# Kernel tuning notes

Measured on AMD Instinct MI355X. Metric: run time of the kernel, lower is better.

Reference implementation:

```python
import jax, jax.numpy as jnp
import numpy as np
import math

B, S, D, H = 32, 512, 1024, 1024


def setup_inputs() -> dict:
    key = jax.random.key(0)
    k_feats, k_wih, k_whh, k_bih, k_bhh = jax.random.split(key, 5)
    stdv = 1.0 / math.sqrt(H)
    u = lambda k, shape: jax.random.uniform(k, shape, jnp.float32, -stdv, stdv)
    return {
        "feats": jax.random.normal(k_feats, (B, S, D), jnp.float32),
        "weight_ih": u(k_wih, (3 * H, D)),
        "weight_hh": u(k_whh, (3 * H, H)),
        "bias_ih": u(k_bih, (3 * H,)),
        "bias_hh": u(k_bhh, (3 * H,)),
    }


def reference(feats, weight_ih, weight_hh, bias_ih, bias_hh):
    b, s, d = feats.shape
    h_dim = weight_hh.shape[1]
    # Precompute input projections for all timesteps in one GEMM: [B,S,3H]
    gi_all = jnp.einsum('bsd,gd->bsg', feats, weight_ih) + bias_ih

    def step(h, gi_t):
        gh = h @ weight_hh.T + bias_hh  # [B,3H]
        i_r, i_i, i_n = jnp.split(gi_t, 3, axis=-1)
        h_r, h_i, h_n = jnp.split(gh, 3, axis=-1)
        resetgate = jax.nn.sigmoid(i_r + h_r)
        inputgate = jax.nn.sigmoid(i_i + h_i)
        newgate = jnp.tanh(i_n + resetgate * h_n)
        hy = newgate + inputgate * (h - newgate)
        return hy, hy

    h0 = jnp.zeros((b, h_dim), feats.dtype)
    h_last, outs = jax.lax.scan(step, h0, jnp.swapaxes(gi_all, 0, 1))  # outs: [S,B,H]
    output = jnp.swapaxes(outs, 0, 1)  # [B,S,H]
    return output, h_last
```

## Files before the change

kernel.cpp:

```cpp
#include <hip/hip_runtime.h>

#define B_  32
#define S_  512
#define D_  1024
#define H_  1024
#define G3  3072

typedef __attribute__((ext_vector_type(8))) short  short8;
typedef __attribute__((ext_vector_type(4))) float  floatx4;

__device__ __forceinline__ unsigned short f2bf(float f) {
    unsigned int u = __builtin_bit_cast(unsigned int, f);
    u = (u + 0x7FFFu + ((u >> 16) & 1u)) >> 16;
    return (unsigned short)u;
}
__device__ __forceinline__ float bf2f(unsigned short h) {
    unsigned int u = ((unsigned int)h) << 16;
    return __builtin_bit_cast(float, u);
}
__device__ __forceinline__ float fsigmoid(float x) {
    float e = __builtin_amdgcn_exp2f(-1.4426950408889634f * x);
    return __builtin_amdgcn_rcpf(1.f + e);
}
__device__ __forceinline__ float ftanh(float x) {
    float e = __builtin_amdgcn_exp2f(2.8853900817779268f * x);
    return 1.f - 2.f * __builtin_amdgcn_rcpf(e + 1.f);
}

__global__ __launch_bounds__(256) void convert_kernel(
    const float* __restrict__ wih, const float* __restrict__ whh,
    unsigned short* __restrict__ wih_h,
    unsigned short* __restrict__ whh_h, unsigned short* __restrict__ whh_l,
    unsigned int* __restrict__ hbuf ,
    int* __restrict__ cnt ) {
    int tid = blockIdx.x * 256 + threadIdx.x;
    int i4 = tid * 4;
    if (i4 < 3145728) {
        float4 w = *(const float4*)(wih + i4);
        ushort4 o;
        o.x = f2bf(w.x); o.y = f2bf(w.y); o.z = f2bf(w.z); o.w = f2bf(w.w);
        *(ushort4*)(wih_h + i4) = o;

        float4 v = *(const float4*)(whh + i4);
        ushort4 h;
        h.x = f2bf(v.x); h.y = f2bf(v.y); h.z = f2bf(v.z); h.w = f2bf(v.w);
        ushort4 l;
        l.x = f2bf(v.x - bf2f(h.x)); l.y = f2bf(v.y - bf2f(h.y));
        l.z = f2bf(v.z - bf2f(h.z)); l.w = f2bf(v.w - bf2f(h.w));
        *(ushort4*)(whh_h + i4) = h;
        *(ushort4*)(whh_l + i4) = l;
    }
    if (tid < 16384) {
        uint4 z; z.x = z.y = z.z = z.w = 0;
        *(uint4*)(hbuf + tid * 4) = z;
    }
    if (tid < 32) {
        int4 z4; z4.x = z4.y = z4.z = z4.w = 0;
        *(int4*)(cnt + tid * 4) = z4;
    }
}

#define BM 128
#define BN 128
#define BK 32
#define LDA 40

__global__ __launch_bounds__(256, 2) void gi_gemm(
    const float* __restrict__ feats,
    const unsigned short* __restrict__ wih_h,
    const float* __restrict__ bias_ih,
    unsigned short* __restrict__ gi) {
    __shared__ unsigned short As[BM * LDA];
    __shared__ unsigned short Bs[BN * LDA];

    int bx = blockIdx.x;
    int nb = bx % (G3 / BN);
    int mb = bx / (G3 / BN);
    int m0 = mb * BM, n0 = nb * BN;
    int tid = threadIdx.x;
    int lane = tid & 63, wave = tid >> 6;
    int quad = lane >> 4, l15 = lane & 15;
    int wm = (wave >> 1) * 64, wn = (wave & 1) * 64;

    floatx4 acc[4][4];
#pragma unroll
    for (int i = 0; i < 4; ++i)
#pragma unroll
        for (int j = 0; j < 4; ++j) acc[i][j] = (floatx4){0.f, 0.f, 0.f, 0.f};

    float bias[4];
#pragma unroll
    for (int j = 0; j < 4; ++j) bias[j] = bias_ih[n0 + wn + j * 16 + l15];

    int srow = tid >> 1, shalf = tid & 1;
    const float* aptr = feats + (size_t)(m0 + srow) * D_ + shalf * 16;
    const unsigned short* bptr = wih_h + (size_t)(n0 + srow) * D_ + shalf * 16;
    unsigned short* as = As + srow * LDA + shalf * 16;
    unsigned short* bs = Bs + srow * LDA + shalf * 16;

    for (int kt = 0; kt < D_ / BK; ++kt) {
        int k0 = kt * BK;
        float4 a0 = *(const float4*)(aptr + k0);
        float4 a1 = *(const float4*)(aptr + k0 + 4);
        float4 a2 = *(const float4*)(aptr + k0 + 8);
        float4 a3 = *(const float4*)(aptr + k0 + 12);
        uint4 bA = *(const uint4*)(bptr + k0);
        uint4 bB = *(const uint4*)(bptr + k0 + 8);

        union { unsigned short u16[16]; uint4 v[2]; } pk;
        pk.u16[0] = f2bf(a0.x);  pk.u16[1] = f2bf(a0.y);
        pk.u16[2] = f2bf(a0.z);  pk.u16[3] = f2bf(a0.w);
        pk.u16[4] = f2bf(a1.x);  pk.u16[5] = f2bf(a1.y);
        pk.u16[6] = f2bf(a1.z);  pk.u16[7] = f2bf(a1.w);
        pk.u16[8] = f2bf(a2.x);  pk.u16[9] = f2bf(a2.y);
        pk.u16[10] = f2bf(a2.z); pk.u16[11] = f2bf(a2.w);
        pk.u16[12] = f2bf(a3.x); pk.u16[13] = f2bf(a3.y);
        pk.u16[14] = f2bf(a3.z); pk.u16[15] = f2bf(a3.w);

        *(uint4*)as = pk.v[0];
        *(uint4*)(as + 8) = pk.v[1];
        *(uint4*)bs = bA;
        *(uint4*)(bs + 8) = bB;
        __syncthreads();

        short8 af[4], bf[4];
#pragma unroll
        for (int i = 0; i < 4; ++i)
            af[i] = *(const short8*)(As + (wm + i * 16 + l15) * LDA + quad * 8);
#pragma unroll
        for (int j = 0; j < 4; ++j)
            bf[j] = *(const short8*)(Bs + (wn + j * 16 + l15) * LDA + quad * 8);
#pragma unroll
        for (int i = 0; i < 4; ++i)
#pragma unroll
            for (int j = 0; j < 4; ++j)
                acc[i][j] = __builtin_amdgcn_mfma_f32_16x16x32_bf16(
                    af[i], bf[j], acc[i][j], 0, 0, 0);
        __syncthreads();
    }

#pragma unroll
    for (int i = 0; i < 4; ++i)
#pragma unroll
        for (int j = 0; j < 4; ++j)
#pragma unroll
            for (int r = 0; r < 4; ++r) {
                int m = m0 + wm + i * 16 + quad * 4 + r;
                int n = n0 + wn + j * 16 + l15;
                gi[(size_t)m * G3 + n] = f2bf(acc[i][j][r] + bias[j]);
            }
}

__global__ __launch_bounds__(512, 2) void gru_rec(
    const unsigned short* __restrict__ gi,
    const unsigned short* __restrict__ whh_h,
    const unsigned short* __restrict__ whh_l,
    const float* __restrict__ bias_hh,
    unsigned int* __restrict__ hbuf,
    int* __restrict__ cnt,
    float* __restrict__ out) {
    __shared__ floatx4 parts[8][3][64];

    int jg = blockIdx.x >> 1, mt = blockIdx.x & 1;
    int tid = threadIdx.x;
    int ks = tid >> 6, lane = tid & 63;
    int quad = lane >> 4, l15 = lane & 15;
    int j = jg * 16 + l15;

    short8 wfh[3][4], wfl[3][4];
#pragma unroll
    for (int g = 0; g < 3; ++g)
#pragma unroll
        for (int ki = 0; ki < 4; ++ki) {
            size_t off = (size_t)(g * H_ + j) * H_ + ks * 128 + ki * 32 + quad * 8;
            wfh[g][ki] = *(const short8*)(whh_h + off);
            wfl[g][ki] = *(const short8*)(whh_l + off);
        }

    float bhh[3] = {0.f, 0.f, 0.f};
    float hreg[4] = {0.f, 0.f, 0.f, 0.f};
    if (ks == 0) {
#pragma unroll
        for (int g = 0; g < 3; ++g) bhh[g] = bias_hh[g * H_ + j];
    }

    const int arow = mt * 16 + l15;
    const int kbase = ks * 128 + quad * 8;
    int* const cbase = cnt + mt * 64;

    for (int t = 0; t < S_; ++t) {
        unsigned short giu[3][4];
        if (ks == 0) {
#pragma unroll
            for (int g = 0; g < 3; ++g)
#pragma unroll
                for (int r = 0; r < 4; ++r) {
                    int b = mt * 16 + quad * 4 + r;
                    giu[g][r] = gi[((size_t)b * S_ + t) * G3 + g * H_ + j];
                }
        }

        if (t > 0) {
            if (ks == 0) {
                int v = __hip_atomic_load(cbase + lane, __ATOMIC_RELAXED,
                                          __HIP_MEMORY_SCOPE_AGENT);
                while (!__all(v >= t)) {
                    __builtin_amdgcn_s_sleep(1);
                    v = __hip_atomic_load(cbase + lane, __ATOMIC_RELAXED,
                                          __HIP_MEMORY_SCOPE_AGENT);
                }
            }
            __syncthreads();
        }

        const unsigned int* hc = hbuf + ((t & 1) << 15);
        unsigned int* hn = hbuf + (((t & 1) ^ 1) << 15);

        unsigned long long q[16];
        {
            const unsigned long long* p =
                (const unsigned long long*)(hc + arow * H_ + kbase);
#pragma unroll
            for (int ki = 0; ki < 4; ++ki)
#pragma unroll
                for (int c = 0; c < 4; ++c)
                    q[ki * 4 + c] = __hip_atomic_load(p + ki * 16 + c,
                                                      __ATOMIC_RELAXED,
                                                      __HIP_MEMORY_SCOPE_AGENT);
        }
        short8 ah[4], al[4];
#pragma unroll
        for (int ki = 0; ki < 4; ++ki) {
            short8 av, lv;
#pragma unroll
            for (int c = 0; c < 4; ++c) {
                unsigned long long qq = q[ki * 4 + c];
                unsigned int u0 = (unsigned int)qq;
                unsigned int u1 = (unsigned int)(qq >> 32);
                av[2 * c]     = (short)(u0 & 0xffffu);
                av[2 * c + 1] = (short)(u1 & 0xffffu);
                lv[2 * c]     = (short)(u0 >> 16);
                lv[2 * c + 1] = (short)(u1 >> 16);
            }
            ah[ki] = av;
            al[ki] = lv;
        }

        floatx4 acc[3];
#pragma unroll
        for (int g = 0; g < 3; ++g) acc[g] = (floatx4){0.f, 0.f, 0.f, 0.f};
#pragma unroll
        for (int ki = 0; ki < 4; ++ki)
#pragma unroll
            for (int g = 0; g < 3; ++g) {
                acc[g] = __builtin_amdgcn_mfma_f32_16x16x32_bf16(ah[ki], wfh[g][ki], acc[g], 0, 0, 0);
                acc[g] = __builtin_amdgcn_mfma_f32_16x16x32_bf16(ah[ki], wfl[g][ki], acc[g], 0, 0, 0);
                acc[g] = __builtin_amdgcn_mfma_f32_16x16x32_bf16(al[ki], wfh[g][ki], acc[g], 0, 0, 0);
            }
#pragma unroll
        for (int g = 0; g < 3; ++g) parts[ks][g][lane] = acc[g];
        __syncthreads();

        float hy[4];
        if (ks == 0) {
            floatx4 gh[3];
#pragma unroll
            for (int g = 0; g < 3; ++g) {
                floatx4 s = parts[0][g][lane];
#pragma unroll
                for (int w = 1; w < 8; ++w) s += parts[w][g][lane];
                gh[g] = s;
            }
#pragma unroll
            for (int r = 0; r < 4; ++r) {
                int b = mt * 16 + quad * 4 + r;
                float rg = fsigmoid(bf2f(giu[0][r]) + gh[0][r] + bhh[0]);
                float zg = fsigmoid(bf2f(giu[1][r]) + gh[1][r] + bhh[1]);
                float ng = ftanh(bf2f(giu[2][r]) + rg * (gh[2][r] + bhh[2]));
                float h = ng + zg * (hreg[r] - ng);
                hreg[r] = h;
                hy[r] = h;
                unsigned short hh = f2bf(h);
                unsigned int pk = (unsigned int)hh |
                                  ((unsigned int)f2bf(h - bf2f(hh)) << 16);
                __hip_atomic_store(hn + b * H_ + j, pk, __ATOMIC_RELAXED,
                                   __HIP_MEMORY_SCOPE_AGENT);
            }
            asm volatile("s_waitcnt vmcnt(0)" ::: "memory");
            if (tid == 0)
                __hip_atomic_store(cbase + jg, t + 1, __ATOMIC_RELAXED,
                                   __HIP_MEMORY_SCOPE_AGENT);
#pragma unroll
            for (int r = 0; r < 4; ++r) {
                int b = mt * 16 + quad * 4 + r;
                __builtin_nontemporal_store(hy[r], out + ((size_t)b * S_ + t) * H_ + j);
                if (t == S_ - 1)
                    __builtin_nontemporal_store(hy[r], out + (size_t)B_ * S_ * H_ + (size_t)b * H_ + j);
            }
        }
    }
}

extern "C" void kernel_launch(void* const* d_in, const int* in_sizes, int n_in,
                              void* d_out, int out_size, void* d_ws, size_t ws_size,
                              hipStream_t stream) {
    const float* feats = (const float*)d_in[0];
    const float* wih   = (const float*)d_in[1];
    const float* whh   = (const float*)d_in[2];
    const float* bih   = (const float*)d_in[3];
    const float* bhh   = (const float*)d_in[4];
    float* out = (float*)d_out;

    unsigned short* wih_h = (unsigned short*)d_ws;
    unsigned short* whh_h = wih_h + (size_t)3145728;
    unsigned short* whh_l = whh_h + (size_t)3145728;
    unsigned short* gi    = whh_l + (size_t)3145728;
    unsigned int*   hbuf  = (unsigned int*)(gi + (size_t)16384 * G3);
    int*            cnt   = (int*)(hbuf + 65536);

    hipLaunchKernelGGL(convert_kernel, dim3(3072), dim3(256), 0, stream,
                       wih, whh, wih_h, whh_h, whh_l, hbuf, cnt);
    hipLaunchKernelGGL(gi_gemm, dim3(3072), dim3(256), 0, stream,
                       feats, wih_h, bih, gi);

    void* args[] = {(void*)&gi, (void*)&whh_h, (void*)&whh_l,
                    (void*)&bhh, (void*)&hbuf, (void*)&cnt, (void*)&out};
    hipLaunchCooperativeKernel((const void*)gru_rec, dim3(128), dim3(512),
                               args, 0, stream);
}
```

Before: 3.435 ms.

## Replace counter barrier with step-tagged hidden-state words and spread gate epilogue

Drops the per-block progress counters and the spin-wait-then-syncthreads handshake. Each hidden-state entry is now stored as a 64-bit word carrying the timestep tag beside the packed bf16 hi/lo value. Consumers poll their own slice until every tag matches, and they do it in two halves so the MFMA inputs for the first half can be ready sooner. The gate epilogue now runs on 256 threads with one element each instead of one wave handling four, and the next step's gi values are prefetched during the current step. The cost is twice the hidden-state traffic per step and an extra __syncthreads.

```diff
diff --git a/kernel.cpp b/kernel.cpp
--- a/kernel.cpp
+++ b/kernel.cpp
@@ -31,8 +31,7 @@
     const float* __restrict__ wih, const float* __restrict__ whh,
     unsigned short* __restrict__ wih_h,
     unsigned short* __restrict__ whh_h, unsigned short* __restrict__ whh_l,
-    unsigned int* __restrict__ hbuf ,
-    int* __restrict__ cnt ) {
+    unsigned int* __restrict__ hbuf ) {
     int tid = blockIdx.x * 256 + threadIdx.x;
     int i4 = tid * 4;
     if (i4 < 3145728) {
@@ -50,13 +49,9 @@
         *(ushort4*)(whh_h + i4) = h;
         *(ushort4*)(whh_l + i4) = l;
     }
-    if (tid < 16384) {
+    if (tid < 32768) {
         uint4 z; z.x = z.y = z.z = z.w = 0;
         *(uint4*)(hbuf + tid * 4) = z;
-    }
-    if (tid < 32) {
-        int4 z4; z4.x = z4.y = z4.z = z4.w = 0;
-        *(int4*)(cnt + tid * 4) = z4;
     }
 }
 
@@ -156,16 +151,15 @@
     const unsigned short* __restrict__ whh_h,
     const unsigned short* __restrict__ whh_l,
     const float* __restrict__ bias_hh,
-    unsigned int* __restrict__ hbuf,
-    int* __restrict__ cnt,
+    unsigned long long* __restrict__ hbuf,
     float* __restrict__ out) {
     __shared__ floatx4 parts[8][3][64];
 
-    int jg = blockIdx.x >> 1, mt = blockIdx.x & 1;
-    int tid = threadIdx.x;
-    int ks = tid >> 6, lane = tid & 63;
-    int quad = lane >> 4, l15 = lane & 15;
-    int j = jg * 16 + l15;
+    const int tid = threadIdx.x;
+    const int lane = tid & 63, ks = tid >> 6;
+    const int quad = lane >> 4, l15 = lane & 15;
+    const int jg = blockIdx.x >> 1, mt = blockIdx.x & 1;
+    const int j = jg * 16 + l15;
 
     short8 wfh[3][4], wfl[3][4];
 #pragma unroll
@@ -177,73 +171,87 @@
             wfl[g][ki] = *(const short8*)(whh_l + off);
         }
 
-    float bhh[3] = {0.f, 0.f, 0.f};
-    float hreg[4] = {0.f, 0.f, 0.f, 0.f};
-    if (ks == 0) {
-#pragma unroll
-        for (int g = 0; g < 3; ++g) bhh[g] = bias_hh[g * H_ + j];
+    const int rr = (tid >> 4) & 15, cc = tid & 15;
+    const int brow = mt * 16 + rr;
+    const int jc = jg * 16 + cc;
+    float bR = 0.f, bZ = 0.f, bN = 0.f, hreg = 0.f;
+    unsigned short giR = 0, giZ = 0, giN = 0;
+    if (tid < 256) {
+        bR = bias_hh[jc]; bZ = bias_hh[H_ + jc]; bN = bias_hh[2 * H_ + jc];
+        const size_t gb = (size_t)brow * S_ * G3 + jc;
+        giR = gi[gb]; giZ = gi[gb + H_]; giN = gi[gb + 2 * H_];
     }
 
     const int arow = mt * 16 + l15;
-    const int kbase = ks * 128 + quad * 8;
-    int* const cbase = cnt + mt * 64;
+    const size_t lslice = (size_t)arow * 1024 + ks * 128 + quad * 8;
+    const float* const pf = (const float*)parts;
 
     for (int t = 0; t < S_; ++t) {
-        unsigned short giu[3][4];
-        if (ks == 0) {
-#pragma unroll
-            for (int g = 0; g < 3; ++g)
-#pragma unroll
-                for (int r = 0; r < 4; ++r) {
-                    int b = mt * 16 + quad * 4 + r;
-                    giu[g][r] = gi[((size_t)b * S_ + t) * G3 + g * H_ + j];
+        const unsigned long long* hp = hbuf + ((size_t)(t & 1) << 15) + lslice;
+        const unsigned int want = (unsigned int)t;
+
+        short8 ah[4], al[4];
+        {
+            unsigned long long q[16];
+            int ok;
+            do {
+#pragma unroll
+                for (int ki = 0; ki < 2; ++ki)
+#pragma unroll
+                    for (int c = 0; c < 8; ++c)
+                        q[ki * 8 + c] = __hip_atomic_load(hp + ki * 32 + c,
+                                                          __ATOMIC_RELAXED,
+                                                          __HIP_MEMORY_SCOPE_AGENT);
+                ok = 1;
+#pragma unroll
+                for (int i = 0; i < 16; ++i)
+                    ok &= ((unsigned int)(q[i] >> 32) == want);
+            } while (!__all(ok));
+#pragma unroll
+            for (int ki = 0; ki < 2; ++ki) {
+                short8 av, lv;
+#pragma unroll
+                for (int c = 0; c < 8; ++c) {
+                    unsigned int d = (unsigned int)q[ki * 8 + c];
+                    av[c] = (short)(d & 0xffffu);
+                    lv[c] = (short)(d >> 16);
                 }
-        }
-
-        if (t > 0) {
-            if (ks == 0) {
-                int v = __hip_atomic_load(cbase + lane, __ATOMIC_RELAXED,
-                                          __HIP_MEMORY_SCOPE_AGENT);
-                while (!__all(v >= t)) {
-                    __builtin_amdgcn_s_sleep(1);
-                    v = __hip_atomic_load(cbase + lane, __ATOMIC_RELAXED,
-                                          __HIP_MEMORY_SCOPE_AGENT);
+                ah[ki] = av; al[ki] = lv;
+            }
+        }
+        {
+            unsigned long long q[16];
+            int ok;
+            do {
+#pragma unroll
+                for (int ki = 0; ki < 2; ++ki)
+#pragma unroll
+                    for (int c = 0; c < 8; ++c)
+                        q[ki * 8 + c] = __hip_atomic_load(hp + (ki + 2) * 32 + c,
+                                                          __ATOMIC_RELAXED,
+                                                          __HIP_MEMORY_SCOPE_AGENT);
+                ok = 1;
+#pragma unroll
+                for (int i = 0; i < 16; ++i)
+                    ok &= ((unsigned int)(q[i] >> 32) == want);
+            } while (!__all(ok));
+#pragma unroll
+            for (int ki = 0; ki < 2; ++ki) {
+                short8 av, lv;
+#pragma unroll
+                for (int c = 0; c < 8; ++c) {
+                    unsigned int d = (unsigned int)q[ki * 8 + c];
+                    av[c] = (short)(d & 0xffffu);
+                    lv[c] = (short)(d >> 16);
                 }
-            }
-            __syncthreads();
-        }
-
-        const unsigned int* hc = hbuf + ((t & 1) << 15);
-        unsigned int* hn = hbuf + (((t & 1) ^ 1) << 15);
-
-        unsigned long long q[16];
-        {
-            const unsigned long long* p =
-                (const unsigned long long*)(hc + arow * H_ + kbase);
-#pragma unroll
-            for (int ki = 0; ki < 4; ++ki)
-#pragma unroll
-                for (int c = 0; c < 4; ++c)
-                    q[ki * 4 + c] = __hip_atomic_load(p + ki * 16 + c,
-                                                      __ATOMIC_RELAXED,
-                                                      __HIP_MEMORY_SCOPE_AGENT);
-        }
-        short8 ah[4], al[4];
-#pragma unroll
-        for (int ki = 0; ki < 4; ++ki) {
-            short8 av, lv;
-#pragma unroll
-            for (int c = 0; c < 4; ++c) {
-                unsigned long long qq = q[ki * 4 + c];
-                unsigned int u0 = (unsigned int)qq;
-                unsigned int u1 = (unsigned int)(qq >> 32);
-                av[2 * c]     = (short)(u0 & 0xffffu);
-                av[2 * c + 1] = (short)(u1 & 0xffffu);
-                lv[2 * c]     = (short)(u0 >> 16);
-                lv[2 * c + 1] = (short)(u1 >> 16);
-            }
-            ah[ki] = av;
-            al[ki] = lv;
+                ah[ki + 2] = av; al[ki + 2] = lv;
+            }
+        }
+
+        unsigned short nR = 0, nZ = 0, nN = 0;
+        if (tid < 256 && t + 1 < S_) {
+            const size_t gb = ((size_t)brow * S_ + (t + 1)) * G3 + jc;
+            nR = gi[gb]; nZ = gi[gb + H_]; nN = gi[gb + 2 * H_];
         }
 
         floatx4 acc[3];
@@ -261,43 +269,39 @@
         for (int g = 0; g < 3; ++g) parts[ks][g][lane] = acc[g];
         __syncthreads();
 
-        float hy[4];
-        if (ks == 0) {
-            floatx4 gh[3];
-#pragma unroll
-            for (int g = 0; g < 3; ++g) {
-                floatx4 s = parts[0][g][lane];
-#pragma unroll
-                for (int w = 1; w < 8; ++w) s += parts[w][g][lane];
-                gh[g] = s;
-            }
-#pragma unroll
-            for (int r = 0; r < 4; ++r) {
-                int b = mt * 16 + quad * 4 + r;
-                float rg = fsigmoid(bf2f(giu[0][r]) + gh[0][r] + bhh[0]);
-                float zg = fsigmoid(bf2f(giu[1][r]) + gh[1][r] + bhh[1]);
-                float ng = ftanh(bf2f(giu[2][r]) + rg * (gh[2][r] + bhh[2]));
-                float h = ng + zg * (hreg[r] - ng);
-                hreg[r] = h;
-                hy[r] = h;
-                unsigned short hh = f2bf(h);
-                unsigned int pk = (unsigned int)hh |
-                                  ((unsigned int)f2bf(h - bf2f(hh)) << 16);
-                __hip_atomic_store(hn + b * H_ + j, pk, __ATOMIC_RELAXED,
-                                   __HIP_MEMORY_SCOPE_AGENT);
-            }
-            asm volatile("s_waitcnt vmcnt(0)" ::: "memory");
-            if (tid == 0)
-                __hip_atomic_store(cbase + jg, t + 1, __ATOMIC_RELAXED,
-                                   __HIP_MEMORY_SCOPE_AGENT);
-#pragma unroll
-            for (int r = 0; r < 4; ++r) {
-                int b = mt * 16 + quad * 4 + r;
-                __builtin_nontemporal_store(hy[r], out + ((size_t)b * S_ + t) * H_ + j);
-                if (t == S_ - 1)
-                    __builtin_nontemporal_store(hy[r], out + (size_t)B_ * S_ * H_ + (size_t)b * H_ + j);
-            }
-        }
+        float gh0 = 0.f, gh1 = 0.f, gh2 = 0.f;
+        if (tid < 256) {
+            const int vidx = ((rr >> 2) * 16 + cc) * 4 + (rr & 3);
+#pragma unroll
+            for (int w = 0; w < 8; ++w) {
+                gh0 += pf[((w * 3 + 0) * 64) * 4 + vidx];
+                gh1 += pf[((w * 3 + 1) * 64) * 4 + vidx];
+                gh2 += pf[((w * 3 + 2) * 64) * 4 + vidx];
+            }
+        }
+        __syncthreads();
+
+        if (tid < 256) {
+            const float rg = fsigmoid(bf2f(giR) + gh0 + bR);
+            const float zg = fsigmoid(bf2f(giZ) + gh1 + bZ);
+            const float ng = ftanh(bf2f(giN) + rg * (gh2 + bN));
+            const float hy = ng + zg * (hreg - ng);
+            hreg = hy;
+            const unsigned short hh = f2bf(hy);
+            const unsigned int pk = (unsigned int)hh |
+                                    ((unsigned int)f2bf(hy - bf2f(hh)) << 16);
+            const unsigned long long hv =
+                ((unsigned long long)(unsigned int)(t + 1) << 32) |
+                (unsigned long long)pk;
+            __hip_atomic_store(hbuf + ((size_t)((t + 1) & 1) << 15) +
+                               (size_t)brow * 1024 + jc,
+                               hv, __ATOMIC_RELAXED, __HIP_MEMORY_SCOPE_AGENT);
+            __builtin_nontemporal_store(hy, out + ((size_t)brow * S_ + t) * H_ + jc);
+            if (t == S_ - 1)
+                __builtin_nontemporal_store(hy,
+                    out + (size_t)B_ * S_ * H_ + (size_t)brow * H_ + jc);
+        }
+        giR = nR; giZ = nZ; giN = nN;
     }
 }
 
@@ -315,16 +319,15 @@
     unsigned short* whh_h = wih_h + (size_t)3145728;
     unsigned short* whh_l = whh_h + (size_t)3145728;
     unsigned short* gi    = whh_l + (size_t)3145728;
-    unsigned int*   hbuf  = (unsigned int*)(gi + (size_t)16384 * G3);
-    int*            cnt   = (int*)(hbuf + 65536);
+    unsigned long long* hbuf = (unsigned long long*)(gi + (size_t)16384 * G3);
 
     hipLaunchKernelGGL(convert_kernel, dim3(3072), dim3(256), 0, stream,
-                       wih, whh, wih_h, whh_h, whh_l, hbuf, cnt);
+                       wih, whh, wih_h, whh_h, whh_l, (unsigned int*)hbuf);
     hipLaunchKernelGGL(gi_gemm, dim3(3072), dim3(256), 0, stream,
                        feats, wih_h, bih, gi);
 
     void* args[] = {(void*)&gi, (void*)&whh_h, (void*)&whh_l,
-                    (void*)&bhh, (void*)&hbuf, (void*)&cnt, (void*)&out};
+                    (void*)&bhh, (void*)&hbuf, (void*)&out};
     hipLaunchCooperativeKernel((const void*)gru_rec, dim3(128), dim3(512),
                                args, 0, stream);
 }
```

New measurement: 5.772 ms. +68.0%, slower.

## Ping-pong two batch halves per block to overlap grid sync with MFMA

Applied to the files above, without the earlier changes.

Each block now owns both 16-row batch halves of its 16 hidden columns, which halves the grid to 64 blocks. It alternates between them: one half's recurrent MFMA runs while the other half's cross-block flag wait is pending, using separate flag arrays and LDS partial buffers. The gate epilogue is spread over 256 threads instead of 64, and output writes are buffered in LDS and flushed every 4 timesteps. Per-block work doubles and is serialized, so the gain depends on hiding spin-wait latency behind the other half's compute.

```diff
diff --git a/kernel.cpp b/kernel.cpp
--- a/kernel.cpp
+++ b/kernel.cpp
@@ -159,13 +159,16 @@
     unsigned int* __restrict__ hbuf,
     int* __restrict__ cnt,
     float* __restrict__ out) {
-    __shared__ floatx4 parts[8][3][64];
-
-    int jg = blockIdx.x >> 1, mt = blockIdx.x & 1;
-    int tid = threadIdx.x;
-    int ks = tid >> 6, lane = tid & 63;
-    int quad = lane >> 4, l15 = lane & 15;
-    int j = jg * 16 + l15;
+    __shared__ floatx4 partsA[8][3][64];
+    __shared__ floatx4 partsB[8][3][64];
+    __shared__ float sbufA[1024];
+    __shared__ float sbufB[1024];
+
+    const int tid = threadIdx.x;
+    const int lane = tid & 63, ks = tid >> 6;
+    const int quad = lane >> 4, l15 = lane & 15;
+    const int jg = blockIdx.x;
+    const int j = jg * 16 + l15;
 
     short8 wfh[3][4], wfl[3][4];
 #pragma unroll
@@ -177,49 +180,36 @@
             wfl[g][ki] = *(const short8*)(whh_l + off);
         }
 
-    float bhh[3] = {0.f, 0.f, 0.f};
-    float hreg[4] = {0.f, 0.f, 0.f, 0.f};
-    if (ks == 0) {
-#pragma unroll
-        for (int g = 0; g < 3; ++g) bhh[g] = bias_hh[g * H_ + j];
-    }
-
-    const int arow = mt * 16 + l15;
+    const int rr = (tid >> 4) & 15, cc = tid & 15;
+    const int browA = rr, browB = 16 + rr;
+    const int jc = jg * 16 + cc;
+    float bR = 0.f, bZ = 0.f, bN = 0.f;
+    float hrA = 0.f, hrB = 0.f;
+    if (tid < 256) {
+        bR = bias_hh[jc]; bZ = bias_hh[H_ + jc]; bN = bias_hh[2 * H_ + jc];
+    }
+
+    int* const fA = cnt;
+    int* const fB = cnt + 64;
     const int kbase = ks * 128 + quad * 8;
-    int* const cbase = cnt + mt * 64;
+    const float* const pfA = (const float*)partsA;
+    const float* const pfB = (const float*)partsB;
 
     for (int t = 0; t < S_; ++t) {
-        unsigned short giu[3][4];
-        if (ks == 0) {
-#pragma unroll
-            for (int g = 0; g < 3; ++g)
-#pragma unroll
-                for (int r = 0; r < 4; ++r) {
-                    int b = mt * 16 + quad * 4 + r;
-                    giu[g][r] = gi[((size_t)b * S_ + t) * G3 + g * H_ + j];
-                }
-        }
-
-        if (t > 0) {
-            if (ks == 0) {
-                int v = __hip_atomic_load(cbase + lane, __ATOMIC_RELAXED,
-                                          __HIP_MEMORY_SCOPE_AGENT);
-                while (!__all(v >= t)) {
-                    __builtin_amdgcn_s_sleep(1);
-                    v = __hip_atomic_load(cbase + lane, __ATOMIC_RELAXED,
-                                          __HIP_MEMORY_SCOPE_AGENT);
-                }
-            }
-            __syncthreads();
-        }
-
         const unsigned int* hc = hbuf + ((t & 1) << 15);
         unsigned int* hn = hbuf + (((t & 1) ^ 1) << 15);
 
-        unsigned long long q[16];
+        unsigned short gAr = 0, gAz = 0, gAn = 0, gBr = 0, gBz = 0, gBn = 0;
+        if (tid < 256) {
+            const size_t gbA = ((size_t)browA * S_ + t) * G3 + jc;
+            const size_t gbB = ((size_t)browB * S_ + t) * G3 + jc;
+            gAr = gi[gbA]; gAz = gi[gbA + H_]; gAn = gi[gbA + 2 * H_];
+            gBr = gi[gbB]; gBz = gi[gbB + H_]; gBn = gi[gbB + 2 * H_];
+        }
         {
+            unsigned long long q[16];
             const unsigned long long* p =
-                (const unsigned long long*)(hc + arow * H_ + kbase);
+                (const unsigned long long*)(hc + (16 + l15) * H_ + kbase);
 #pragma unroll
             for (int ki = 0; ki < 4; ++ki)
 #pragma unroll
@@ -227,77 +217,172 @@
                     q[ki * 4 + c] = __hip_atomic_load(p + ki * 16 + c,
                                                       __ATOMIC_RELAXED,
                                                       __HIP_MEMORY_SCOPE_AGENT);
-        }
-        short8 ah[4], al[4];
-#pragma unroll
-        for (int ki = 0; ki < 4; ++ki) {
-            short8 av, lv;
-#pragma unroll
-            for (int c = 0; c < 4; ++c) {
-                unsigned long long qq = q[ki * 4 + c];
-                unsigned int u0 = (unsigned int)qq;
-                unsigned int u1 = (unsigned int)(qq >> 32);
-                av[2 * c]     = (short)(u0 & 0xffffu);
-                av[2 * c + 1] = (short)(u1 & 0xffffu);
-                lv[2 * c]     = (short)(u0 >> 16);
-                lv[2 * c + 1] = (short)(u1 >> 16);
-            }
-            ah[ki] = av;
-            al[ki] = lv;
-        }
-
-        floatx4 acc[3];
-#pragma unroll
-        for (int g = 0; g < 3; ++g) acc[g] = (floatx4){0.f, 0.f, 0.f, 0.f};
-#pragma unroll
-        for (int ki = 0; ki < 4; ++ki)
-#pragma unroll
-            for (int g = 0; g < 3; ++g) {
-                acc[g] = __builtin_amdgcn_mfma_f32_16x16x32_bf16(ah[ki], wfh[g][ki], acc[g], 0, 0, 0);
-                acc[g] = __builtin_amdgcn_mfma_f32_16x16x32_bf16(ah[ki], wfl[g][ki], acc[g], 0, 0, 0);
-                acc[g] = __builtin_amdgcn_mfma_f32_16x16x32_bf16(al[ki], wfh[g][ki], acc[g], 0, 0, 0);
-            }
-#pragma unroll
-        for (int g = 0; g < 3; ++g) parts[ks][g][lane] = acc[g];
-        __syncthreads();
-
-        float hy[4];
-        if (ks == 0) {
-            floatx4 gh[3];
-#pragma unroll
-            for (int g = 0; g < 3; ++g) {
-                floatx4 s = parts[0][g][lane];
-#pragma unroll
-                for (int w = 1; w < 8; ++w) s += parts[w][g][lane];
-                gh[g] = s;
-            }
-#pragma unroll
-            for (int r = 0; r < 4; ++r) {
-                int b = mt * 16 + quad * 4 + r;
-                float rg = fsigmoid(bf2f(giu[0][r]) + gh[0][r] + bhh[0]);
-                float zg = fsigmoid(bf2f(giu[1][r]) + gh[1][r] + bhh[1]);
-                float ng = ftanh(bf2f(giu[2][r]) + rg * (gh[2][r] + bhh[2]));
-                float h = ng + zg * (hreg[r] - ng);
-                hreg[r] = h;
-                hy[r] = h;
-                unsigned short hh = f2bf(h);
-                unsigned int pk = (unsigned int)hh |
-                                  ((unsigned int)f2bf(h - bf2f(hh)) << 16);
-                __hip_atomic_store(hn + b * H_ + j, pk, __ATOMIC_RELAXED,
-                                   __HIP_MEMORY_SCOPE_AGENT);
-            }
+            short8 ah[4], al[4];
+#pragma unroll
+            for (int ki = 0; ki < 4; ++ki) {
+                short8 av, lv;
+#pragma unroll
+                for (int c = 0; c < 4; ++c) {
+                    unsigned long long qq = q[ki * 4 + c];
+                    unsigned int u0 = (unsigned int)qq;
+                    unsigned int u1 = (unsigned int)(qq >> 32);
+                    av[2 * c]     = (short)(u0 & 0xffffu);
+                    av[2 * c + 1] = (short)(u1 & 0xffffu);
+                    lv[2 * c]     = (short)(u0 >> 16);
+                    lv[2 * c + 1] = (short)(u1 >> 16);
+                }
+                ah[ki] = av; al[ki] = lv;
+            }
+            floatx4 acc[3];
+#pragma unroll
+            for (int g = 0; g < 3; ++g) acc[g] = (floatx4){0.f, 0.f, 0.f, 0.f};
+#pragma unroll
+            for (int ki = 0; ki < 4; ++ki)
+#pragma unroll
+                for (int g = 0; g < 3; ++g) {
+                    acc[g] = __builtin_amdgcn_mfma_f32_16x16x32_bf16(ah[ki], wfh[g][ki], acc[g], 0, 0, 0);
+                    acc[g] = __builtin_amdgcn_mfma_f32_16x16x32_bf16(ah[ki], wfl[g][ki], acc[g], 0, 0, 0);
+                    acc[g] = __builtin_amdgcn_mfma_f32_16x16x32_bf16(al[ki], wfh[g][ki], acc[g], 0, 0, 0);
+                }
+#pragma unroll
+            for (int g = 0; g < 3; ++g) partsB[ks][g][lane] = acc[g];
+        }
+        __syncthreads();
+
+        if (ks == 4) {
+            int v = __hip_atomic_load(fA + lane, __ATOMIC_RELAXED,
+                                      __HIP_MEMORY_SCOPE_AGENT);
+            while (!__all(v >= t)) {
+                __builtin_amdgcn_s_sleep(1);
+                v = __hip_atomic_load(fA + lane, __ATOMIC_RELAXED,
+                                      __HIP_MEMORY_SCOPE_AGENT);
+            }
+        }
+        if (tid < 256) {
+            const int lidx = ((rr >> 2) * 16 + cc);
+            const int r4 = rr & 3;
+            float gh0 = 0.f, gh1 = 0.f, gh2 = 0.f;
+#pragma unroll
+            for (int w = 0; w < 8; ++w) {
+                gh0 += pfB[(((w * 3 + 0) * 64 + lidx) << 2) + r4];
+                gh1 += pfB[(((w * 3 + 1) * 64 + lidx) << 2) + r4];
+                gh2 += pfB[(((w * 3 + 2) * 64 + lidx) << 2) + r4];
+            }
+            const float rg = fsigmoid(bf2f(gBr) + gh0 + bR);
+            const float zg = fsigmoid(bf2f(gBz) + gh1 + bZ);
+            const float ng = ftanh(bf2f(gBn) + rg * (gh2 + bN));
+            const float hy = ng + zg * (hrB - ng);
+            hrB = hy;
+            const unsigned short hh = f2bf(hy);
+            const unsigned int pk = (unsigned int)hh |
+                                    ((unsigned int)f2bf(hy - bf2f(hh)) << 16);
+            __hip_atomic_store(hn + browB * H_ + jc, pk, __ATOMIC_RELAXED,
+                               __HIP_MEMORY_SCOPE_AGENT);
             asm volatile("s_waitcnt vmcnt(0)" ::: "memory");
             if (tid == 0)
-                __hip_atomic_store(cbase + jg, t + 1, __ATOMIC_RELAXED,
+                __hip_atomic_store(fB + jg, t + 1, __ATOMIC_RELAXED,
                                    __HIP_MEMORY_SCOPE_AGENT);
-#pragma unroll
-            for (int r = 0; r < 4; ++r) {
-                int b = mt * 16 + quad * 4 + r;
-                __builtin_nontemporal_store(hy[r], out + ((size_t)b * S_ + t) * H_ + j);
-                if (t == S_ - 1)
-                    __builtin_nontemporal_store(hy[r], out + (size_t)B_ * S_ * H_ + (size_t)b * H_ + j);
-            }
-        }
+            sbufB[(t & 3) * 256 + tid] = hy;
+            if ((t & 3) == 3) {
+#pragma unroll
+                for (int i = 0; i < 4; ++i)
+                    __builtin_nontemporal_store(sbufB[i * 256 + tid],
+                        out + ((size_t)browB * S_ + (t - 3 + i)) * H_ + jc);
+            }
+            if (t == S_ - 1)
+                __builtin_nontemporal_store(hrB,
+                    out + (size_t)B_ * S_ * H_ + (size_t)browB * H_ + jc);
+        }
+        __syncthreads();
+
+        {
+            unsigned long long q[16];
+            const unsigned long long* p =
+                (const unsigned long long*)(hc + l15 * H_ + kbase);
+#pragma unroll
+            for (int ki = 0; ki < 4; ++ki)
+#pragma unroll
+                for (int c = 0; c < 4; ++c)
+                    q[ki * 4 + c] = __hip_atomic_load(p + ki * 16 + c,
+                                                      __ATOMIC_RELAXED,
+                                                      __HIP_MEMORY_SCOPE_AGENT);
+            short8 ah[4], al[4];
+#pragma unroll
+            for (int ki = 0; ki < 4; ++ki) {
+                short8 av, lv;
+#pragma unroll
+                for (int c = 0; c < 4; ++c) {
+                    unsigned long long qq = q[ki * 4 + c];
+                    unsigned int u0 = (unsigned int)qq;
+                    unsigned int u1 = (unsigned int)(qq >> 32);
+                    av[2 * c]     = (short)(u0 & 0xffffu);
+                    av[2 * c + 1] = (short)(u1 & 0xffffu);
+                    lv[2 * c]     = (short)(u0 >> 16);
+                    lv[2 * c + 1] = (short)(u1 >> 16);
+                }
+                ah[ki] = av; al[ki] = lv;
+            }
+            floatx4 acc[3];
+#pragma unroll
+            for (int g = 0; g < 3; ++g) acc[g] = (floatx4){0.f, 0.f, 0.f, 0.f};
+#pragma unroll
+            for (int ki = 0; ki < 4; ++ki)
+#pragma unroll
+                for (int g = 0; g < 3; ++g) {
+                    acc[g] = __builtin_amdgcn_mfma_f32_16x16x32_bf16(ah[ki], wfh[g][ki], acc[g], 0, 0, 0);
+                    acc[g] = __builtin_amdgcn_mfma_f32_16x16x32_bf16(ah[ki], wfl[g][ki], acc[g], 0, 0, 0);
+                    acc[g] = __builtin_amdgcn_mfma_f32_16x16x32_bf16(al[ki], wfh[g][ki], acc[g], 0, 0, 0);
+                }
+#pragma unroll
+            for (int g = 0; g < 3; ++g) partsA[ks][g][lane] = acc[g];
+        }
+        __syncthreads();
+
+        if (ks == 4 && t + 1 < S_) {
+            int v = __hip_atomic_load(fB + lane, __ATOMIC_RELAXED,
+                                      __HIP_MEMORY_SCOPE_AGENT);
+            while (!__all(v >= t + 1)) {
+                __builtin_amdgcn_s_sleep(1);
+                v = __hip_atomic_load(fB + lane, __ATOMIC_RELAXED,
+                                      __HIP_MEMORY_SCOPE_AGENT);
+            }
+        }
+        if (tid < 256) {
+            const int lidx = ((rr >> 2) * 16 + cc);
+            const int r4 = rr & 3;
+            float gh0 = 0.f, gh1 = 0.f, gh2 = 0.f;
+#pragma unroll
+            for (int w = 0; w < 8; ++w) {
+                gh0 += pfA[(((w * 3 + 0) * 64 + lidx) << 2) + r4];
+                gh1 += pfA[(((w * 3 + 1) * 64 + lidx) << 2) + r4];
+                gh2 += pfA[(((w * 3 + 2) * 64 + lidx) << 2) + r4];
+            }
+            const float rg = fsigmoid(bf2f(gAr) + gh0 + bR);
+            const float zg = fsigmoid(bf2f(gAz) + gh1 + bZ);
+            const float ng = ftanh(bf2f(gAn) + rg * (gh2 + bN));
+            const float hy = ng + zg * (hrA - ng);
+            hrA = hy;
+            const unsigned short hh = f2bf(hy);
+            const unsigned int pk = (unsigned int)hh |
+                                    ((unsigned int)f2bf(hy - bf2f(hh)) << 16);
+            __hip_atomic_store(hn + browA * H_ + jc, pk, __ATOMIC_RELAXED,
+                               __HIP_MEMORY_SCOPE_AGENT);
+            asm volatile("s_waitcnt vmcnt(0)" ::: "memory");
+            if (tid == 0)
+                __hip_atomic_store(fA + jg, t + 1, __ATOMIC_RELAXED,
+                                   __HIP_MEMORY_SCOPE_AGENT);
+            sbufA[(t & 3) * 256 + tid] = hy;
+            if ((t & 3) == 3) {
+#pragma unroll
+                for (int i = 0; i < 4; ++i)
+                    __builtin_nontemporal_store(sbufA[i * 256 + tid],
+                        out + ((size_t)browA * S_ + (t - 3 + i)) * H_ + jc);
+            }
+            if (t == S_ - 1)
+                __builtin_nontemporal_store(hrA,
+                    out + (size_t)B_ * S_ * H_ + (size_t)browA * H_ + jc);
+        }
+        __syncthreads();
     }
 }
 
@@ -325,6 +410,6 @@
 
     void* args[] = {(void*)&gi, (void*)&whh_h, (void*)&whh_l,
                     (void*)&bhh, (void*)&hbuf, (void*)&cnt, (void*)&out};
-    hipLaunchCooperativeKernel((const void*)gru_rec, dim3(128), dim3(512),
+    hipLaunchCooperativeKernel((const void*)gru_rec, dim3(64), dim3(512),
                                args, 0, stream);
 }
```

New measurement: 5.248 ms. 52.8% more time.
